# Kernel optimization log

Hardware: AMD Instinct MI355X
Metric: run time of the kernel (lower is better)

## Reference

```python
import jax, jax.numpy as jnp
import numpy as np

H, W = 180, 330
SIZE = 36
K = SIZE + 1  # gaussian patch is 37x37 (arange(-18, 19))
SIGMA = 3.0
XR = (30.0, 31.0)
YR = (120.0, 122.0)
ALPHA = 0.7
EPS = 1e-4


def _conv(x, w, b):
    # 3x3 stride-1 'same' conv, NCHW / OIHW
    y = jax.lax.conv_general_dilated(x, w, (1, 1), 'SAME',
                                     dimension_numbers=('NCHW', 'OIHW', 'NCHW'))
    return y + b[None, :, None, None]


def _bn(x, g, b):
    # eval-mode batchnorm with running_mean=0, running_var=1
    return x * g[None, :, None, None] + b[None, :, None, None]


def _pool(x):
    return jax.lax.reduce_window(x, -jnp.inf, jax.lax.max,
                                 (1, 1, 2, 2), (1, 1, 2, 2), 'VALID')


def _heatmap(x_t):
    # vectorized gaussian splatting (replaces the torch double python loop)
    B, T = x_t.shape[0], x_t.shape[1]
    x_scale = H / (XR[1] - XR[0])
    y_scale = W / (YR[1] - YR[0])
    xp = H - ((x_t[:, :, 0] - XR[0]) * x_scale).astype(jnp.int32)  # [B,T]
    yp = ((x_t[:, :, 1] - YR[0]) * y_scale).astype(jnp.int32)
    valid = ~(jnp.isnan(x_t[:, :, 0]) | jnp.isnan(x_t[:, :, 1]))

    ax = jnp.arange(-(SIZE // 2), SIZE // 2 + 1, dtype=jnp.float32)  # 37
    k1 = jnp.exp(-ax ** 2 / (2.0 * SIGMA ** 2))
    kern = k1[:, None] * k1[None, :]
    kern = kern / kern.sum()  # [K,K]

    xs = jnp.clip(xp - SIZE // 2, 0, H - SIZE)
    xe = jnp.clip(xp + SIZE // 2, 0, H)
    ys = jnp.clip(yp - SIZE // 2, 0, W - SIZE)
    ye = jnp.clip(yp + SIZE // 2, 0, W)

    r = jnp.arange(K)
    # mask = kernel[:ksx, :ksy] selection, matching torch's top-left slicing
    mask = (r[None, None, :, None] < (xe - xs)[:, :, None, None]) \
         & (r[None, None, None, :] < (ye - ys)[:, :, None, None]) \
         & valid[:, :, None, None]
    patch = kern[None, None] * mask  # [B,T,K,K]

    # scatter-add into padded heatmap, then crop
    Hp, Wp = H + K, W + K
    bidx = jnp.arange(B)[:, None, None, None]
    ridx = xs[:, :, None, None] + r[None, None, :, None]
    cidx = ys[:, :, None, None] + r[None, None, None, :]
    idx = (bidx * Hp + ridx) * Wp + cidx  # [B,T,K,K]
    heat = jnp.zeros((B * Hp * Wp,), jnp.float32)
    heat = heat.at[idx.reshape(-1)].add(patch.reshape(-1))
    heat = heat.reshape(B, Hp, Wp)[:, :H, :W]

    m = heat.max(axis=(1, 2), keepdims=True)
    return heat / (m + 1e-10)


def reference(x_t, image_tensor,
              c1_w, c1_b, bn1_g, bn1_b, c2_w, c2_b, bn2_g, bn2_b,
              a1_w, a1_b, abn1_g, abn1_b, a2_w, a2_b, abn2_g, abn2_b,
              p1_w, p1_b, pbn1_g, pbn1_b, p2_w, p2_b, pbn2_g, pbn2_b,
              fc_w, fc_b):
    heat = _heatmap(x_t)
    fused = ALPHA * heat + (1.0 - ALPHA) * image_tensor  # [B,H,W]
    x = fused[:, None]  # [B,1,H,W]

    # features
    x = _pool(jax.nn.relu(_bn(_conv(x, c1_w, c1_b), bn1_g, bn1_b)))   # [B,32,90,165]
    x = _pool(jax.nn.relu(_bn(_conv(x, c2_w, c2_b), bn2_g, bn2_b)))   # [B,64,45,82]

    # add_ons -> f_x
    f = jax.nn.relu(_bn(_conv(x, a1_w, a1_b), abn1_g, abn1_b))
    f_x = jax.nn.sigmoid(_bn(_conv(f, a2_w, a2_b), abn2_g, abn2_b))   # [B,128,45,82]

    # get_p_map: p_map[:-1] (conv,bn,relu,conv,bn) then relu, scale, steep sigmoid
    p = jax.nn.relu(_bn(_conv(x, p1_w, p1_b), pbn1_g, pbn1_b))
    p = jax.nn.relu(_bn(_conv(p, p2_w, p2_b), pbn2_g, pbn2_b))
    p = p - p.min(axis=(1, 2, 3), keepdims=True)
    p = p / jnp.maximum(p.max(axis=(1, 2, 3), keepdims=True), EPS)
    p_map = jax.nn.sigmoid(10.0 * (p - 0.5))                          # [B,128,45,82]

    # attn_map + fc1
    p_size = f_x.shape[2] * f_x.shape[3]
    p_x = jnp.einsum('bphw,bchw->bpc', p_map, f_x) / p_size           # [B,128,128]
    out = p_x.reshape(p_x.shape[0], -1) @ fc_w.T + fc_b               # [B,256]
    return out


def setup_inputs() -> dict:
    key = jax.random.key(0)
    ks = jax.random.split(key, 32)
    B, T = 32, 1024
    u = jax.random.uniform(ks[0], (B, T, 2))
    x_t = jnp.stack([XR[0] + u[..., 0] * (XR[1] - XR[0]),
                     YR[0] + u[..., 1] * (YR[1] - YR[0])], axis=-1)
    image_tensor = jax.random.uniform(ks[1], (B, H, W))

    def w(k, shp):
        return jax.random.normal(k, shp, jnp.float32) * 0.05

    inp = {'x_t': x_t, 'image_tensor': image_tensor,
           'c1_w': w(ks[2], (32, 1, 3, 3)), 'c1_b': w(ks[3], (32,)),
           'bn1_g': jnp.ones((32,)), 'bn1_b': w(ks[4], (32,)),
           'c2_w': w(ks[5], (64, 32, 3, 3)), 'c2_b': w(ks[6], (64,)),
           'bn2_g': jnp.ones((64,)), 'bn2_b': w(ks[7], (64,)),
           'a1_w': w(ks[8], (128, 64, 3, 3)), 'a1_b': w(ks[9], (128,)),
           'abn1_g': jnp.ones((128,)), 'abn1_b': w(ks[10], (128,)),
           'a2_w': w(ks[11], (128, 128, 3, 3)), 'a2_b': w(ks[12], (128,)),
           'abn2_g': jnp.ones((128,)), 'abn2_b': w(ks[13], (128,)),
           'p1_w': w(ks[14], (128, 64, 3, 3)), 'p1_b': w(ks[15], (128,)),
           'pbn1_g': jnp.ones((128,)), 'pbn1_b': w(ks[16], (128,)),
           'p2_w': w(ks[17], (128, 128, 3, 3)), 'p2_b': w(ks[18], (128,)),
           'pbn2_g': jnp.ones((128,)), 'pbn2_b': w(ks[19], (128,)),
           'fc_w': w(ks[20], (256, 16384)), 'fc_b': w(ks[21], (256,))}
    return inp
```

## Files before the change

### kernel.cpp

```cpp
#include <hip/hip_runtime.h>
#include <hip/hip_bf16.h>

#define NB 32
#define NT 1024
#define IH 180
#define IW 330
#define KSZ 37
#define XBINS 181
#define H1 90
#define W1 165
#define H2 45
#define W2 82
#define PIX2 (H2*W2)
#define KTOT PIX2
#define KPAD 3712
#define CH1 32
#define CH2 64
#define CH3 128
#define NSTRIP 6
#define NKC 8

#define NKF 256
#define KCF 64

#define BXR 12
#define YHW 165
#define GROWS_MAX 54

#define EL_HEAT (IH*IW)
#define EL_REGB 237600
#define EL_REGC (CH2*PIX2/2)
#define EL_REGD (CH3*KPAD/2)
#define EL_REGE (CH3*KPAD/2)
#define EL_PX   (CH3*CH3)
#define EL_PER_BATCH (EL_HEAT + EL_REGB + EL_REGC + EL_REGD + EL_REGE + EL_PX)

#define WSH_A1 (9*128*64)
#define WSH_A2 (9*128*128)
#define WSH_C2 (9*64*32)
#define WSH_TOT (2*WSH_A1 + 2*WSH_A2 + WSH_C2)

typedef __attribute__((ext_vector_type(8))) short short8;
typedef __attribute__((ext_vector_type(4))) float floatx4;

__device__ __forceinline__ short f2bf(float v) {
    __hip_bfloat16 h = __float2bfloat16(v);
    return *reinterpret_cast<short*>(&h);
}
__device__ __forceinline__ float b2f(short s) {
    __hip_bfloat16 h = *reinterpret_cast<__hip_bfloat16*>(&s);
    return __bfloat162float(h);
}

__global__ __launch_bounds__(256) void mm_init(unsigned* __restrict__ m_bits,
                                               unsigned* __restrict__ pmm_bits) {
    int i = threadIdx.x;
    if (i < 64) {
        m_bits[i] = 0u;
        pmm_bits[2 * i]     = 0x7F800000u;
        pmm_bits[2 * i + 1] = 0u;
    }
}

__global__ __launch_bounds__(256) void heat_scatter_cols(const float* __restrict__ x_t,
                                                         float* __restrict__ G,
                                                         int b0) {
    const int strip = blockIdx.x;
    const int lb = blockIdx.y;
    const int b = b0 + lb;
    const int c0 = strip * 64;
    const int cw = min(64, IW - c0);
    __shared__ float g[XBINS * 64];
    __shared__ float k1n[64];
    __shared__ float2 pts[NT];
    const int tid = threadIdx.x;

    if (tid < 64) {
        float v = 0.0f;
        if (tid < KSZ) {
            float ax = (float)tid - 18.0f;
            v = expf(-ax * ax / 18.0f);
        }
        k1n[tid] = v;
    }
    for (int i = tid; i < XBINS * 64; i += 256) g[i] = 0.0f;
    {
        const float2* xb = (const float2*)x_t + (size_t)b * NT;
        for (int i = tid; i < NT; i += 256) pts[i] = xb[i];
    }
    __syncthreads();
    if (tid == 0) {
        float s = 0.0f;
        for (int i = 0; i < KSZ; i++) s += k1n[i];
        float inv = 1.0f / s;
        for (int i = 0; i < KSZ; i++) k1n[i] *= inv;
    }
    __syncthreads();

    const int wave = tid >> 6;
    const int lane = tid & 63;
    const float kc = k1n[lane];

    for (int p = wave; p < NT; p += 4) {
        float x = pts[p].x, y = pts[p].y;
        if (isnan(x) || isnan(y)) continue;
        int xp = IH - (int)((x - 30.0f) * 180.0f);
        xp = min(max(xp, 0), 180);
        int yp = (int)((y - 120.0f) * 165.0f);
        int ys = min(max(yp - 18, 0), IW - 36);
        int ye = min(max(yp + 18, 0), IW);
        int nc = ye - ys;
        int col = ys + lane;
        if (lane < nc && col >= c0 && col < c0 + cw)
            atomicAdd(&g[xp * 64 + col - c0], kc);
    }
    __syncthreads();
    for (int i = tid; i < XBINS * cw; i += 256) {
        int row = i / cw, col = i % cw;
        G[((size_t)lb * XBINS + row) * IW + c0 + col] = g[row * 64 + col];
    }
}

__global__ __launch_bounds__(256) void heat_rowcombine(const float* __restrict__ G,
                                                       float* __restrict__ heat,
                                                       unsigned* __restrict__ m_bits) {
    const int band = blockIdx.x;
    const int lb = blockIdx.y;
    const int half = blockIdx.z;
    const int X0 = band * BXR;
    const int c0 = half * YHW;
    const int tid = threadIdx.x;

    __shared__ float k1n[64];
    __shared__ float gs[GROWS_MAX * YHW];
    __shared__ float red[256];

    if (tid < 64) {
        float v = 0.0f;
        if (tid < KSZ) {
            float ax = (float)tid - 18.0f;
            v = expf(-ax * ax / 18.0f);
        }
        k1n[tid] = v;
    }

    const int rlo = max(0, X0 - 17);
    const int rhi = (X0 + BXR - 1 >= IH - 36) ? 180 : (X0 + BXR - 1 + 18);
    const int nrows = rhi - rlo + 1;
    const float* Gb = G + (size_t)lb * XBINS * IW;
    for (int i = tid; i < nrows * YHW; i += 256) {
        int r = i / YHW, y = i % YHW;
        gs[i] = Gb[(size_t)(rlo + r) * IW + c0 + y];
    }
    __syncthreads();
    if (tid == 0) {
        float s = 0.0f;
        for (int i = 0; i < KSZ; i++) s += k1n[i];
        float inv = 1.0f / s;
        for (int i = 0; i < KSZ; i++) k1n[i] *= inv;
    }
    __syncthreads();

    float lmax = 0.0f;
    for (int p = tid; p < BXR * YHW; p += 256) {
        const int xr = p / YHW;
        const int yy = p % YHW;
        const int X = X0 + xr;
        const int Y = c0 + yy;
        const int lo = max(0, X - 17);
        const int hi = (X >= IH - 36) ? 180 : X + 18;
        float s = 0.0f;
        for (int xp = lo; xp <= hi; ++xp) {
            int xs = min(max(xp - 18, 0), IH - 36);
            s += k1n[X - xs] * gs[(xp - rlo) * YHW + yy];
        }
        heat[(size_t)lb * EL_HEAT + (size_t)X * IW + Y] = s;
        lmax = fmaxf(lmax, s);
    }
    red[tid] = lmax;
    __syncthreads();
    for (int st = 128; st > 0; st >>= 1) {
        if (tid < st) red[tid] = fmaxf(red[tid], red[tid + st]);
        __syncthreads();
    }
    if (tid == 0) atomicMax(&m_bits[lb], __float_as_uint(red[0]));
}

__global__ __launch_bounds__(256) void conv1_pool(const float* __restrict__ heat,
                                                  const float* __restrict__ image,
                                                  const float* __restrict__ m,
                                                  const float* __restrict__ w,
                                                  const float* __restrict__ cb,
                                                  const float* __restrict__ g,
                                                  const float* __restrict__ bb,
                                                  short* __restrict__ out1,
                                                  int b0, int gb) {
    __shared__ float ws_[CH1 * 9];
    __shared__ float bs_[CH1];
    const int tid = threadIdx.x;
    for (int i = tid; i < CH1 * 9; i += 256) {
        int oc = i / 9;
        ws_[i] = w[i] * g[oc];
    }
    if (tid < CH1) bs_[tid] = cb[tid] * g[tid] + bb[tid];
    __syncthreads();

    int t = blockIdx.x * 256 + tid;
    if (t >= gb * H1 * W1) return;
    int lb = t / (H1 * W1);
    int r = t % (H1 * W1);
    int py = r / W1, px = r % W1;
    const float s = 0.7f / (m[lb] + 1e-10f);
    const float* hb = heat + (size_t)lb * EL_HEAT;
    const float* ib = image + (size_t)(b0 + lb) * EL_HEAT;

    float v[4][4];
    int y0 = 2 * py - 1, x0 = 2 * px - 1;
#pragma unroll
    for (int i = 0; i < 4; i++) {
#pragma unroll
        for (int j = 0; j < 4; j++) {
            int y = y0 + i, x = x0 + j;
            float val = 0.0f;
            if (y >= 0 && y < IH && x >= 0 && x < IW) {
                size_t idx = (size_t)y * IW + x;
                val = s * hb[idx] + 0.3f * ib[idx];
            }
            v[i][j] = val;
        }
    }
    short8 pk[4];
#pragma unroll
    for (int oc = 0; oc < CH1; oc++) {
        float a00 = 0, a01 = 0, a10 = 0, a11 = 0;
        const float* wp = &ws_[oc * 9];
#pragma unroll
        for (int ky = 0; ky < 3; ky++) {
#pragma unroll
            for (int kx = 0; kx < 3; kx++) {
                float wv = wp[ky * 3 + kx];
                a00 += wv * v[ky][kx];
                a01 += wv * v[ky][kx + 1];
                a10 += wv * v[ky + 1][kx];
                a11 += wv * v[ky + 1][kx + 1];
            }
        }
        float bias = bs_[oc];
        a00 = fmaxf(a00 + bias, 0.0f);
        a01 = fmaxf(a01 + bias, 0.0f);
        a10 = fmaxf(a10 + bias, 0.0f);
        a11 = fmaxf(a11 + bias, 0.0f);
        pk[oc >> 3][oc & 7] = f2bf(fmaxf(fmaxf(a00, a01), fmaxf(a10, a11)));
    }
    short8* op = reinterpret_cast<short8*>(&out1[((size_t)lb * H1 * W1 + r) * CH1]);
#pragma unroll
    for (int vv = 0; vv < 4; vv++) op[vv] = pk[vv];
}

__global__ __launch_bounds__(256) void wfold_k(const float* __restrict__ w,
                                               const float* __restrict__ g,
                                               const float* __restrict__ cb,
                                               const float* __restrict__ bb,
                                               short* __restrict__ wT,
                                               float* __restrict__ bfold,
                                               int OC, int IC) {
    int i = blockIdx.x * 256 + threadIdx.x;
    int n = 9 * OC * IC;
    if (i >= n) return;
    int tap = i / (OC * IC);
    int r = i % (OC * IC);
    int oc = r / IC;
    int ic = r % IC;
    wT[i] = f2bf(w[((size_t)oc * IC + ic) * 9 + tap] * g[oc]);
    if (tap == 0 && ic == 0) bfold[oc] = cb[oc] * g[oc] + bb[oc];
}

__global__ __launch_bounds__(256) void conv2_mfma(const short* __restrict__ in,
                                                  const short* __restrict__ wT,
                                                  const float* __restrict__ bfold,
                                                  short* __restrict__ out) {
    const int xt = blockIdx.x;
    const int yt = blockIdx.y;
    const int lb = blockIdx.z;
    const int x0 = xt * 32, y0 = yt * 8;
    const int tid = threadIdx.x;
    const int wave = tid >> 6, lane = tid & 63;
    const int mm = lane & 15, q = lane >> 4;
    constexpr int AP = 40;
    constexpr int CP = 72;
    __shared__ __align__(16) short smem[10 * 34 * AP];

    floatx4 acc[2][2][4];
#pragma unroll
    for (int a = 0; a < 2; ++a)
#pragma unroll
        for (int bq = 0; bq < 2; ++bq)
#pragma unroll
            for (int j = 0; j < 4; ++j) acc[a][bq][j] = (floatx4){0.f, 0.f, 0.f, 0.f};

    const short* inb = in + (size_t)lb * (H1 * W1) * CH1;
    for (int e = tid; e < 10 * 34 * 4; e += 256) {
        int dy = e / (34 * 4);
        int r = e % (34 * 4);
        int tx = r / 4;
        int i8 = r % 4;
        int yin = y0 + dy - 1, xin = x0 + tx - 1;
        short8 hv = {0, 0, 0, 0, 0, 0, 0, 0};
        if (yin >= 0 && yin < H1 && xin >= 0 && xin < W1)
            hv = *reinterpret_cast<const short8*>(&inb[((size_t)(yin * W1 + xin)) * CH1 + i8 * 8]);
        *reinterpret_cast<short8*>(&smem[(dy * 34 + tx) * AP + i8 * 8]) = hv;
    }
    __syncthreads();

#pragma unroll
    for (int tap = 0; tap < 9; ++tap) {
        const int dy = tap / 3, dx = tap % 3;
        short8 bf[4];
#pragma unroll
        for (int j = 0; j < 4; ++j)
            bf[j] = *reinterpret_cast<const short8*>(&wT[((size_t)tap * 64 + j * 16 + mm) * 32 + q * 8]);
#pragma unroll
        for (int row = 0; row < 2; ++row) {
#pragma unroll
            for (int xh = 0; xh < 2; ++xh) {
                short8 af = *reinterpret_cast<const short8*>(
                    &smem[((2 * wave + row + dy) * 34 + xh * 16 + dx + mm) * AP + q * 8]);
#pragma unroll
                for (int j = 0; j < 4; ++j)
                    acc[row][xh][j] = __builtin_amdgcn_mfma_f32_16x16x32_bf16(af, bf[j], acc[row][xh][j], 0, 0, 0);
            }
        }
    }
    __syncthreads();

    short* cst = smem;
#pragma unroll
    for (int xh = 0; xh < 2; ++xh) {
#pragma unroll
        for (int j = 0; j < 4; ++j) {
            const float bias = bfold[j * 16 + mm];
#pragma unroll
            for (int rp = 0; rp < 2; ++rp) {
                int pxl = xh * 8 + q * 2 + rp;
                float v = fmaxf(fmaxf(acc[0][xh][j][2 * rp], acc[0][xh][j][2 * rp + 1]),
                                fmaxf(acc[1][xh][j][2 * rp], acc[1][xh][j][2 * rp + 1]));
                v = fmaxf(v + bias, 0.0f);
                cst[(wave * 16 + pxl) * CP + j * 16 + mm] = f2bf(v);
            }
        }
    }
    __syncthreads();

    short* ob = out + (size_t)lb * PIX2 * CH2;
    for (int e = tid; e < 512; e += 256) {
        int pl = e >> 3, c8 = e & 7;
        int py = yt * 4 + (pl >> 4);
        int pxg = xt * 16 + (pl & 15);
        if (py < H2 && pxg < W2)
            *reinterpret_cast<short8*>(&ob[((size_t)py * W2 + pxg) * CH2 + c8 * 8]) =
                *reinterpret_cast<const short8*>(&cst[pl * CP + c8 * 8]);
    }
}

template <int IC, bool SIG, int OM>
__global__ __launch_bounds__(256) void conv3x3_mfma(const short* __restrict__ in,
                                                    const short* __restrict__ wT,
                                                    const float* __restrict__ bfold,
                                                    short* __restrict__ outp) {
    const int xt = blockIdx.x;
    const int yt = blockIdx.y;
    const int lb = blockIdx.z;
    const int x0 = xt * 32, y0 = yt * 4;
    const int tid = threadIdx.x;
    const int wave = tid >> 6, lane = tid & 63;
    const int mm = lane & 15, q = lane >> 4;

    constexpr int KC = 32;
    constexpr int NCH = IC / KC;
    constexpr int AP = 40;
    constexpr int CP0 = 136;
    constexpr int CP2 = 132;
    __shared__ __align__(16) short smem[17408];

    floatx4 acc[16];
#pragma unroll
    for (int i = 0; i < 16; ++i) acc[i] = (floatx4){0.f, 0.f, 0.f, 0.f};

    const short* inb = in + (size_t)lb * PIX2 * IC;

    for (int c = 0; c < NCH; ++c) {
        const int ic0 = c * KC;
        for (int e = tid; e < 6 * 34 * (KC / 8); e += 256) {
            int dy = e / (34 * (KC / 8));
            int r  = e % (34 * (KC / 8));
            int tx = r / (KC / 8);
            int i8 = r % (KC / 8);
            int yin = y0 + dy - 1, xin = x0 + tx - 1;
            short8 hv = {0, 0, 0, 0, 0, 0, 0, 0};
            if (yin >= 0 && yin < H2 && xin >= 0 && xin < W2)
                hv = *reinterpret_cast<const short8*>(
                    &inb[((size_t)(yin * W2 + xin)) * IC + ic0 + i8 * 8]);
            *reinterpret_cast<short8*>(&smem[(dy * 34 + tx) * AP + i8 * 8]) = hv;
        }
        __syncthreads();

        const int oc0 = wave * 32 + mm;
#pragma unroll
        for (int tap = 0; tap < 9; ++tap) {
            const int dy = tap / 3, dx = tap % 3;
            short8 b0 = *reinterpret_cast<const short8*>(
                &wT[((size_t)tap * 128 + oc0) * IC + ic0 + q * 8]);
            short8 b1 = *reinterpret_cast<const short8*>(
                &wT[((size_t)tap * 128 + oc0 + 16) * IC + ic0 + q * 8]);
#pragma unroll
            for (int t = 0; t < 8; ++t) {
                const int tr = t >> 1, tc = t & 1;
                short8 af = *reinterpret_cast<const short8*>(
                    &smem[((tr + dy) * 34 + tc * 16 + dx + mm) * AP + q * 8]);
                acc[t * 2]     = __builtin_amdgcn_mfma_f32_16x16x32_bf16(af, b0, acc[t * 2], 0, 0, 0);
                acc[t * 2 + 1] = __builtin_amdgcn_mfma_f32_16x16x32_bf16(af, b1, acc[t * 2 + 1], 0, 0, 0);
            }
        }
        __syncthreads();
    }

    const int oc0 = wave * 32 + mm;
    const float bias0 = bfold[oc0];
    const float bias1 = bfold[oc0 + 16];
    short* cst = smem;
#pragma unroll
    for (int t = 0; t < 8; ++t) {
        const int tr = t >> 1, tc = t & 1;
#pragma unroll
        for (int r = 0; r < 4; ++r) {
            int pl = tr * 32 + tc * 16 + q * 4 + r;
            float z0 = acc[t * 2][r] + bias0;
            float z1 = acc[t * 2 + 1][r] + bias1;
            if (SIG) {
                z0 = 1.0f / (1.0f + expf(-z0));
                z1 = 1.0f / (1.0f + expf(-z1));
            } else {
                z0 = fmaxf(z0, 0.0f);
                z1 = fmaxf(z1, 0.0f);
            }
            if (OM == 0) {
                cst[pl * CP0 + oc0] = f2bf(z0);
                cst[pl * CP0 + oc0 + 16] = f2bf(z1);
            } else {
                cst[oc0 * CP2 + pl] = f2bf(z0);
                cst[(oc0 + 16) * CP2 + pl] = f2bf(z1);
            }
        }
    }
    __syncthreads();

    if (OM == 0) {
        short* ob = outp + (size_t)lb * PIX2 * 128;
        for (int e = tid; e < 2048; e += 256) {
            int pl = e >> 4, c8 = e & 15;
            int yy = y0 + (pl >> 5), xx = x0 + (pl & 31);
            if (yy < H2 && xx < W2)
                *reinterpret_cast<short8*>(&ob[((size_t)yy * W2 + xx) * 128 + c8 * 8]) =
                    *reinterpret_cast<const short8*>(&cst[pl * CP0 + c8 * 8]);
        }
    } else {
        short* ob = outp + (size_t)lb * 128 * KPAD;
        for (int e = tid; e < 8192; e += 256) {
            int oc = e >> 6;
            int r2 = e & 63;
            int yy4 = r2 >> 4;
            int x2 = (r2 & 15) * 2;
            int yy = y0 + yy4, xx = x0 + x2;
            if (yy < H2 && xx < W2) {
                int pl = yy4 * 32 + x2;
                if (xx + 1 < W2) {
                    *reinterpret_cast<int*>(&ob[(size_t)oc * KPAD + yy * W2 + xx]) =
                        *reinterpret_cast<const int*>(&cst[oc * CP2 + pl]);
                } else {
                    ob[(size_t)oc * KPAD + yy * W2 + xx] = cst[oc * CP2 + pl];
                }
            }
        }
    }
}

__global__ __launch_bounds__(256) void pminmax(const short* __restrict__ p,
                                               unsigned* __restrict__ pmm_bits) {
    const int c = blockIdx.x;
    const int lb = blockIdx.y;
    const short* pb = p + (size_t)lb * 128 * KPAD + (size_t)c * KPAD;
    float mn = INFINITY, mx = 0.0f;
    for (int i = threadIdx.x; i < PIX2; i += 256) {
        float v = b2f(pb[i]);
        mn = fminf(mn, v);
        mx = fmaxf(mx, v);
    }
    __shared__ float rmn[256], rmx[256];
    rmn[threadIdx.x] = mn; rmx[threadIdx.x] = mx;
    __syncthreads();
    for (int s = 128; s > 0; s >>= 1) {
        if (threadIdx.x < s) {
            rmn[threadIdx.x] = fminf(rmn[threadIdx.x], rmn[threadIdx.x + s]);
            rmx[threadIdx.x] = fmaxf(rmx[threadIdx.x], rmx[threadIdx.x + s]);
        }
        __syncthreads();
    }
    if (threadIdx.x == 0) {
        atomicMin(&pmm_bits[lb * 2],     __float_as_uint(rmn[0]));
        atomicMax(&pmm_bits[lb * 2 + 1], __float_as_uint(rmx[0]));
    }
}

__global__ __launch_bounds__(256) void einsum_part(const short* __restrict__ pp2,
                                                   const short* __restrict__ fxb,
                                                   const float* __restrict__ mm_,
                                                   float* __restrict__ px_part) {
    const int kc = blockIdx.x;
    const int lb = blockIdx.y;
    const int gb = gridDim.y;
    const int tid = threadIdx.x;
    const int wave = tid >> 6, lane = tid & 63;
    const int mm = lane & 15, q = lane >> 4;
    constexpr int AP = 72;
    __shared__ __align__(16) short As[128 * AP];
    __shared__ __align__(16) short Bs[128 * AP];

    const float mn = mm_[lb * 2];
    const float denom = fmaxf(mm_[lb * 2 + 1] - mn, 1e-4f);
    const float rden = 1.0f / denom;

    floatx4 acc[2][8];
#pragma unroll
    for (int a = 0; a < 2; ++a)
#pragma unroll
        for (int n = 0; n < 8; ++n) acc[a][n] = (floatx4){0.f, 0.f, 0.f, 0.f};

    const short* Ab = pp2 + (size_t)lb * 128 * KPAD;
    const short* Bb = fxb + (size_t)lb * 128 * KPAD;

    for (int it = 0; it < 8; ++it) {
        const int kk = kc * 512 + it * 64;
        if (kk >= KTOT) break;
        for (int e = tid; e < 2048; e += 256) {
            const bool isA = (e < 1024);
            const int e2 = isA ? e : e - 1024;
            const int row = e2 >> 3, i8 = e2 & 7;
            const int k = kk + i8 * 8;
            const short* src = (isA ? Ab : Bb) + (size_t)row * KPAD + k;
            short8 v = {0, 0, 0, 0, 0, 0, 0, 0};
            if (k + 8 <= KTOT) {
                v = *reinterpret_cast<const short8*>(src);
            } else {
#pragma unroll
                for (int j = 0; j < 8; ++j) v[j] = (k + j < KTOT) ? src[j] : (short)0;
            }
            if (isA) {
#pragma unroll
                for (int j = 0; j < 8; ++j) {
                    if (k + j < KTOT) {
                        float f = (b2f(v[j]) - mn) * rden;
                        v[j] = f2bf(1.0f / (1.0f + expf(-10.0f * (f - 0.5f))));
                    } else v[j] = 0;
                }
                *reinterpret_cast<short8*>(&As[row * AP + i8 * 8]) = v;
            } else {
                *reinterpret_cast<short8*>(&Bs[row * AP + i8 * 8]) = v;
            }
        }
        __syncthreads();
#pragma unroll
        for (int ks = 0; ks < 2; ++ks) {
            short8 af0 = *reinterpret_cast<const short8*>(&As[((2 * wave) * 16 + mm) * AP + ks * 32 + q * 8]);
            short8 af1 = *reinterpret_cast<const short8*>(&As[((2 * wave + 1) * 16 + mm) * AP + ks * 32 + q * 8]);
#pragma unroll
            for (int n = 0; n < 8; ++n) {
                short8 bf = *reinterpret_cast<const short8*>(&Bs[(n * 16 + mm) * AP + ks * 32 + q * 8]);
                acc[0][n] = __builtin_amdgcn_mfma_f32_16x16x32_bf16(af0, bf, acc[0][n], 0, 0, 0);
                acc[1][n] = __builtin_amdgcn_mfma_f32_16x16x32_bf16(af1, bf, acc[1][n], 0, 0, 0);
            }
        }
        __syncthreads();
    }

    float* base = px_part + ((size_t)kc * gb + lb) * EL_PX;
#pragma unroll
    for (int a = 0; a < 2; ++a) {
        const int gm0 = (2 * wave + a) * 16 + q * 4;
#pragma unroll
        for (int n = 0; n < 8; ++n) {
            const int gn = n * 16 + mm;
#pragma unroll
            for (int r = 0; r < 4; ++r)
                base[(size_t)(gm0 + r) * 128 + gn] = acc[a][n][r];
        }
    }
}

__global__ __launch_bounds__(256) void px_reduce(const float* __restrict__ part,
                                                 float* __restrict__ px,
                                                 int gb) {
    int i = blockIdx.x * 256 + threadIdx.x;
    if (i >= gb * EL_PX) return;
    int lb = i / EL_PX;
    int r = i % EL_PX;
    float s = 0.0f;
#pragma unroll
    for (int kc = 0; kc < NKC; ++kc)
        s += part[((size_t)kc * gb + lb) * EL_PX + r];
    px[i] = s * (1.0f / (float)KTOT);
}

__global__ __launch_bounds__(256) void fc_wt(const float* __restrict__ w,
                                             float* __restrict__ wT) {
    __shared__ float t[32][33];
    const int bk = blockIdx.x * 32;
    const int bo = blockIdx.y * 32;
    const int tx = threadIdx.x & 31;
    const int ty = threadIdx.x >> 5;
#pragma unroll
    for (int r = 0; r < 4; ++r) {
        int o = bo + ty + r * 8;
        t[ty + r * 8][tx] = w[(size_t)o * EL_PX + bk + tx];
    }
    __syncthreads();
#pragma unroll
    for (int r = 0; r < 4; ++r) {
        int k = bk + ty + r * 8;
        wT[(size_t)k * 256 + bo + tx] = t[tx][ty + r * 8];
    }
}

__global__ __launch_bounds__(256) void fc_part(const float* __restrict__ px,
                                               const float* __restrict__ wT,
                                               float* __restrict__ part) {
    const int kc = blockIdx.x;
    const int o = threadIdx.x;
    const int k0 = kc * KCF;
    float acc[32];
#pragma unroll
    for (int lb = 0; lb < 32; ++lb) acc[lb] = 0.0f;

    for (int k8 = 0; k8 < KCF; k8 += 8) {
        float wv[8];
#pragma unroll
        for (int j = 0; j < 8; ++j)
            wv[j] = wT[(size_t)(k0 + k8 + j) * 256 + o];
#pragma unroll
        for (int lb = 0; lb < 32; ++lb) {
            const float* pc = px + (size_t)lb * EL_PX + k0 + k8;
            float4 p0 = *reinterpret_cast<const float4*>(pc);
            float4 p1 = *reinterpret_cast<const float4*>(pc + 4);
            acc[lb] += wv[0] * p0.x + wv[1] * p0.y + wv[2] * p0.z + wv[3] * p0.w
                     + wv[4] * p1.x + wv[5] * p1.y + wv[6] * p1.z + wv[7] * p1.w;
        }
    }
    float* pb = part + (size_t)kc * (32 * 256);
#pragma unroll
    for (int lb = 0; lb < 32; ++lb)
        pb[lb * 256 + o] = acc[lb];
}

__global__ __launch_bounds__(256) void fc_out(const float* __restrict__ part,
                                              const float* __restrict__ fcb,
                                              float* __restrict__ out) {
    const int i = blockIdx.x * 256 + threadIdx.x;
    float s = 0.0f;
    for (int c = 0; c < NKF; ++c)
        s += part[(size_t)c * 8192 + i];
    out[i] = s + fcb[i & 255];
}

__global__ __launch_bounds__(256) void fc_k(const float* __restrict__ px,
                                            const float* __restrict__ w,
                                            const float* __restrict__ bias,
                                            float* __restrict__ out,
                                            int b0) {
    const int gw = blockIdx.x * 4 + (threadIdx.x >> 6);
    const int lane = threadIdx.x & 63;
    const int lb = gw >> 8;
    const int o = gw & 255;
    const float* xb = px + (size_t)lb * EL_PX;
    const float* wr = w + (size_t)o * EL_PX;
    float s = 0.0f;
    for (int k = lane; k < EL_PX; k += 64) s += xb[k] * wr[k];
#pragma unroll
    for (int off = 32; off > 0; off >>= 1) s += __shfl_down(s, off);
    if (lane == 0) out[(size_t)(b0 + lb) * 256 + o] = s + bias[o];
}

extern "C" void kernel_launch(void* const* d_in, const int* in_sizes, int n_in,
                              void* d_out, int out_size, void* d_ws, size_t ws_size,
                              hipStream_t stream) {
    const float* x_t   = (const float*)d_in[0];
    const float* image = (const float*)d_in[1];
    const float* c1_w  = (const float*)d_in[2];
    const float* c1_b  = (const float*)d_in[3];
    const float* bn1_g = (const float*)d_in[4];
    const float* bn1_b = (const float*)d_in[5];
    const float* c2_w  = (const float*)d_in[6];
    const float* c2_b  = (const float*)d_in[7];
    const float* bn2_g = (const float*)d_in[8];
    const float* bn2_b = (const float*)d_in[9];
    const float* a1_w  = (const float*)d_in[10];
    const float* a1_b  = (const float*)d_in[11];
    const float* abn1_g= (const float*)d_in[12];
    const float* abn1_b= (const float*)d_in[13];
    const float* a2_w  = (const float*)d_in[14];
    const float* a2_b  = (const float*)d_in[15];
    const float* abn2_g= (const float*)d_in[16];
    const float* abn2_b= (const float*)d_in[17];
    const float* p1_w  = (const float*)d_in[18];
    const float* p1_b  = (const float*)d_in[19];
    const float* pbn1_g= (const float*)d_in[20];
    const float* pbn1_b= (const float*)d_in[21];
    const float* p2_w  = (const float*)d_in[22];
    const float* p2_b  = (const float*)d_in[23];
    const float* pbn2_g= (const float*)d_in[24];
    const float* pbn2_b= (const float*)d_in[25];
    const float* fc_w  = (const float*)d_in[26];
    const float* fc_b  = (const float*)d_in[27];
    float* outp = (float*)d_out;

    float* ws = (float*)d_ws;
    short* wTa1 = (short*)ws;
    short* wTa2 = wTa1 + WSH_A1;
    short* wTp1 = wTa2 + WSH_A2;
    short* wTp2 = wTp1 + WSH_A1;
    short* wTc2 = wTp2 + WSH_A2;
    float* bfa1 = ws + WSH_TOT / 2;
    float* bfa2 = bfa1 + 128;
    float* bfp1 = bfa2 + 128;
    float* bfp2 = bfp1 + 128;
    float* bfc2 = bfp2 + 128;
    float* dyn  = bfc2 + 128;
    const size_t fixed_floats = WSH_TOT / 2 + 1024;

    int GB = 32;
    while (GB > 1) {
        size_t need = ((size_t)GB * EL_PER_BATCH + fixed_floats + 256) * sizeof(float);
        if (need <= ws_size) break;
        GB >>= 1;
    }
    const int ngroups = NB / GB;

    float* heat = dyn;
    float* m    = heat + (size_t)GB * EL_HEAT;
    float* regB = m + 64;
    float* regC = regB + (size_t)GB * EL_REGB;
    float* regD = regC + (size_t)GB * EL_REGC;
    float* regE = regD + (size_t)GB * EL_REGD;
    float* pmm  = regE + (size_t)GB * EL_REGE;
    float* px   = pmm + 128;

    float* G      = regD;
    short* out1b  = (short*)regB;
    short* out2b  = (short*)regC;
    short* fbuf   = (short*)regD;
    short* fxbf   = (short*)regE;
    short* pp1    = (short*)regB;
    short* pp2    = (short*)regD;
    float* pxpart = regB;
    float* fcwT   = regD;
    float* fcpart = regB;

    wfold_k<<<(9 * 128 * CH2 + 255) / 256, 256, 0, stream>>>(a1_w, abn1_g, a1_b, abn1_b, wTa1, bfa1, 128, CH2);
    wfold_k<<<(9 * 128 * CH3 + 255) / 256, 256, 0, stream>>>(a2_w, abn2_g, a2_b, abn2_b, wTa2, bfa2, 128, CH3);
    wfold_k<<<(9 * 128 * CH2 + 255) / 256, 256, 0, stream>>>(p1_w, pbn1_g, p1_b, pbn1_b, wTp1, bfp1, 128, CH2);
    wfold_k<<<(9 * 128 * CH3 + 255) / 256, 256, 0, stream>>>(p2_w, pbn2_g, p2_b, pbn2_b, wTp2, bfp2, 128, CH3);
    wfold_k<<<(9 * 64 * 32 + 255) / 256, 256, 0, stream>>>(c2_w, bn2_g, c2_b, bn2_b, wTc2, bfc2, 64, 32);

    for (int gidx = 0; gidx < ngroups; ++gidx) {
        const int b0 = gidx * GB;
        mm_init<<<1, 256, 0, stream>>>((unsigned*)m, (unsigned*)pmm);
        heat_scatter_cols<<<dim3(NSTRIP, GB), 256, 0, stream>>>(x_t, G, b0);
        heat_rowcombine<<<dim3(IH / BXR, GB, 2), 256, 0, stream>>>(G, heat, (unsigned*)m);
        conv1_pool<<<(GB * H1 * W1 + 255) / 256, 256, 0, stream>>>(
            heat, image, m, c1_w, c1_b, bn1_g, bn1_b, out1b, b0, GB);
        conv2_mfma<<<dim3(6, 12, GB), 256, 0, stream>>>(out1b, wTc2, bfc2, out2b);
        conv3x3_mfma<CH2, false, 0><<<dim3(3, 12, GB), 256, 0, stream>>>(out2b, wTa1, bfa1, fbuf);
        conv3x3_mfma<CH3, true,  2><<<dim3(3, 12, GB), 256, 0, stream>>>(fbuf, wTa2, bfa2, fxbf);
        conv3x3_mfma<CH2, false, 0><<<dim3(3, 12, GB), 256, 0, stream>>>(out2b, wTp1, bfp1, pp1);
        conv3x3_mfma<CH3, false, 2><<<dim3(3, 12, GB), 256, 0, stream>>>(pp1, wTp2, bfp2, pp2);
        pminmax<<<dim3(128, GB), 256, 0, stream>>>(pp2, (unsigned*)pmm);
        einsum_part<<<dim3(NKC, GB), 256, 0, stream>>>(pp2, fxbf, pmm, pxpart);
        px_reduce<<<(GB * EL_PX + 255) / 256, 256, 0, stream>>>(pxpart, px, GB);
        if (GB == 32) {
            fc_wt<<<dim3(EL_PX / 32, 256 / 32), 256, 0, stream>>>(fc_w, fcwT);
            fc_part<<<NKF, 256, 0, stream>>>(px, fcwT, fcpart);
            fc_out<<<8192 / 256, 256, 0, stream>>>(fcpart, fc_b, outp);
        } else {
            fc_k<<<GB * 64, 256, 0, stream>>>(px, fc_w, fc_b, outp, b0);
        }
    }
}
```

Before: 673.3 us.

## Split conv3x3 output channels across blocks and merge twin first-stage convs

Rewrites the 3x3 MFMA conv so each block computes 64 of the 128 output channels, and each wave computes one output row against four weight fragments instead of all rows against two. This doubles the grid (and quadruples it for the merged launch), cuts accumulator registers from 16 to 8 floatx4 and halves shared memory, which should raise occupancy. The two convolutions that read the same input (a1 and p1) are fused into one dual-weight launch, saving a kernel launch. The cost is that the input tile is now loaded into shared memory once per channel half, roughly doubling input halo traffic.

```diff
diff --git a/kernel.cpp b/kernel.cpp
--- a/kernel.cpp
+++ b/kernel.cpp
@@ -362,29 +362,41 @@
     }
 }
 
-template <int IC, bool SIG, int OM>
-__global__ __launch_bounds__(256) void conv3x3_mfma(const short* __restrict__ in,
-                                                    const short* __restrict__ wT,
-                                                    const float* __restrict__ bfold,
-                                                    short* __restrict__ outp) {
+template <int IC, bool SIG, int OM, bool DUAL>
+__global__ __launch_bounds__(256) void conv3x3_v2(const short* __restrict__ in,
+                                                  const short* __restrict__ wA,
+                                                  const short* __restrict__ wB,
+                                                  const float* __restrict__ bA,
+                                                  const float* __restrict__ bB,
+                                                  short* __restrict__ oA,
+                                                  short* __restrict__ oB) {
     const int xt = blockIdx.x;
-    const int yt = blockIdx.y;
+    const int yt = blockIdx.y % 12;
+    const int och = blockIdx.y / 12;
     const int lb = blockIdx.z;
     const int x0 = xt * 32, y0 = yt * 4;
     const int tid = threadIdx.x;
     const int wave = tid >> 6, lane = tid & 63;
     const int mm = lane & 15, q = lane >> 4;
 
+    const short* wT = wA;
+    const float* bfold = bA;
+    short* outp = oA;
+    if (DUAL && och >= 2) { wT = wB; bfold = bB; outp = oB; }
+    const int ocbase = (DUAL ? (och & 1) : och) * 64;
+
     constexpr int KC = 32;
     constexpr int NCH = IC / KC;
     constexpr int AP = 40;
-    constexpr int CP0 = 136;
+    constexpr int CP0 = 72;
     constexpr int CP2 = 132;
-    __shared__ __align__(16) short smem[17408];
-
-    floatx4 acc[16];
-#pragma unroll
-    for (int i = 0; i < 16; ++i) acc[i] = (floatx4){0.f, 0.f, 0.f, 0.f};
+    __shared__ __align__(16) short smem[9216];
+
+    floatx4 acc[2][4];
+#pragma unroll
+    for (int tc = 0; tc < 2; ++tc)
+#pragma unroll
+        for (int j = 0; j < 4; ++j) acc[tc][j] = (floatx4){0.f, 0.f, 0.f, 0.f};
 
     const short* inb = in + (size_t)lb * PIX2 * IC;
 
@@ -404,51 +416,42 @@
         }
         __syncthreads();
 
-        const int oc0 = wave * 32 + mm;
 #pragma unroll
         for (int tap = 0; tap < 9; ++tap) {
             const int dy = tap / 3, dx = tap % 3;
-            short8 b0 = *reinterpret_cast<const short8*>(
-                &wT[((size_t)tap * 128 + oc0) * IC + ic0 + q * 8]);
-            short8 b1 = *reinterpret_cast<const short8*>(
-                &wT[((size_t)tap * 128 + oc0 + 16) * IC + ic0 + q * 8]);
-#pragma unroll
-            for (int t = 0; t < 8; ++t) {
-                const int tr = t >> 1, tc = t & 1;
+            short8 bf[4];
+#pragma unroll
+            for (int j = 0; j < 4; ++j)
+                bf[j] = *reinterpret_cast<const short8*>(
+                    &wT[((size_t)tap * 128 + ocbase + j * 16 + mm) * IC + ic0 + q * 8]);
+#pragma unroll
+            for (int tc = 0; tc < 2; ++tc) {
                 short8 af = *reinterpret_cast<const short8*>(
-                    &smem[((tr + dy) * 34 + tc * 16 + dx + mm) * AP + q * 8]);
-                acc[t * 2]     = __builtin_amdgcn_mfma_f32_16x16x32_bf16(af, b0, acc[t * 2], 0, 0, 0);
-                acc[t * 2 + 1] = __builtin_amdgcn_mfma_f32_16x16x32_bf16(af, b1, acc[t * 2 + 1], 0, 0, 0);
+                    &smem[((wave + dy) * 34 + tc * 16 + dx + mm) * AP + q * 8]);
+#pragma unroll
+                for (int j = 0; j < 4; ++j)
+                    acc[tc][j] = __builtin_amdgcn_mfma_f32_16x16x32_bf16(af, bf[j], acc[tc][j], 0, 0, 0);
             }
         }
         __syncthreads();
     }
 
-    const int oc0 = wave * 32 + mm;
-    const float bias0 = bfold[oc0];
-    const float bias1 = bfold[oc0 + 16];
+    float biasv[4];
+#pragma unroll
+    for (int j = 0; j < 4; ++j) biasv[j] = bfold[ocbase + j * 16 + mm];
     short* cst = smem;
 #pragma unroll
-    for (int t = 0; t < 8; ++t) {
-        const int tr = t >> 1, tc = t & 1;
-#pragma unroll
-        for (int r = 0; r < 4; ++r) {
-            int pl = tr * 32 + tc * 16 + q * 4 + r;
-            float z0 = acc[t * 2][r] + bias0;
-            float z1 = acc[t * 2 + 1][r] + bias1;
-            if (SIG) {
-                z0 = 1.0f / (1.0f + expf(-z0));
-                z1 = 1.0f / (1.0f + expf(-z1));
-            } else {
-                z0 = fmaxf(z0, 0.0f);
-                z1 = fmaxf(z1, 0.0f);
-            }
-            if (OM == 0) {
-                cst[pl * CP0 + oc0] = f2bf(z0);
-                cst[pl * CP0 + oc0 + 16] = f2bf(z1);
-            } else {
-                cst[oc0 * CP2 + pl] = f2bf(z0);
-                cst[(oc0 + 16) * CP2 + pl] = f2bf(z1);
+    for (int tc = 0; tc < 2; ++tc) {
+#pragma unroll
+        for (int j = 0; j < 4; ++j) {
+#pragma unroll
+            for (int r = 0; r < 4; ++r) {
+                int pl = wave * 32 + tc * 16 + q * 4 + r;
+                float z = acc[tc][j][r] + biasv[j];
+                if (SIG) z = 1.0f / (1.0f + expf(-z));
+                else z = fmaxf(z, 0.0f);
+                if (OM == 0) cst[pl * CP0 + j * 16 + mm] = f2bf(z);
+                else cst[(j * 16 + mm) * CP2 + pl] = f2bf(z);
             }
         }
     }
@@ -456,28 +459,29 @@
 
     if (OM == 0) {
         short* ob = outp + (size_t)lb * PIX2 * 128;
-        for (int e = tid; e < 2048; e += 256) {
-            int pl = e >> 4, c8 = e & 15;
+        for (int e = tid; e < 1024; e += 256) {
+            int pl = e >> 3, c8 = e & 7;
             int yy = y0 + (pl >> 5), xx = x0 + (pl & 31);
             if (yy < H2 && xx < W2)
-                *reinterpret_cast<short8*>(&ob[((size_t)yy * W2 + xx) * 128 + c8 * 8]) =
+                *reinterpret_cast<short8*>(&ob[((size_t)yy * W2 + xx) * 128 + ocbase + c8 * 8]) =
                     *reinterpret_cast<const short8*>(&cst[pl * CP0 + c8 * 8]);
         }
     } else {
         short* ob = outp + (size_t)lb * 128 * KPAD;
-        for (int e = tid; e < 8192; e += 256) {
-            int oc = e >> 6;
+        for (int e = tid; e < 4096; e += 256) {
+            int ocl = e >> 6;
             int r2 = e & 63;
             int yy4 = r2 >> 4;
             int x2 = (r2 & 15) * 2;
             int yy = y0 + yy4, xx = x0 + x2;
             if (yy < H2 && xx < W2) {
                 int pl = yy4 * 32 + x2;
+                int oc = ocbase + ocl;
                 if (xx + 1 < W2) {
                     *reinterpret_cast<int*>(&ob[(size_t)oc * KPAD + yy * W2 + xx]) =
-                        *reinterpret_cast<const int*>(&cst[oc * CP2 + pl]);
+                        *reinterpret_cast<const int*>(&cst[ocl * CP2 + pl]);
                 } else {
-                    ob[(size_t)oc * KPAD + yy * W2 + xx] = cst[oc * CP2 + pl];
+                    ob[(size_t)oc * KPAD + yy * W2 + xx] = cst[ocl * CP2 + pl];
                 }
             }
         }
@@ -777,10 +781,12 @@
         conv1_pool<<<(GB * H1 * W1 + 255) / 256, 256, 0, stream>>>(
             heat, image, m, c1_w, c1_b, bn1_g, bn1_b, out1b, b0, GB);
         conv2_mfma<<<dim3(6, 12, GB), 256, 0, stream>>>(out1b, wTc2, bfc2, out2b);
-        conv3x3_mfma<CH2, false, 0><<<dim3(3, 12, GB), 256, 0, stream>>>(out2b, wTa1, bfa1, fbuf);
-        conv3x3_mfma<CH3, true,  2><<<dim3(3, 12, GB), 256, 0, stream>>>(fbuf, wTa2, bfa2, fxbf);
-        conv3x3_mfma<CH2, false, 0><<<dim3(3, 12, GB), 256, 0, stream>>>(out2b, wTp1, bfp1, pp1);
-        conv3x3_mfma<CH3, false, 2><<<dim3(3, 12, GB), 256, 0, stream>>>(pp1, wTp2, bfp2, pp2);
+        conv3x3_v2<CH2, false, 0, true><<<dim3(3, 48, GB), 256, 0, stream>>>(
+            out2b, wTa1, wTp1, bfa1, bfp1, fbuf, pp1);
+        conv3x3_v2<CH3, true,  2, false><<<dim3(3, 24, GB), 256, 0, stream>>>(
+            fbuf, wTa2, wTa2, bfa2, bfa2, fxbf, fxbf);
+        conv3x3_v2<CH3, false, 2, false><<<dim3(3, 24, GB), 256, 0, stream>>>(
+            pp1, wTp2, wTp2, bfp2, bfp2, pp2, pp2);
         pminmax<<<dim3(128, GB), 256, 0, stream>>>(pp2, (unsigned*)pmm);
         einsum_part<<<dim3(NKC, GB), 256, 0, stream>>>(pp2, fxbf, pmm, pxpart);
         px_reduce<<<(GB * EL_PX + 255) / 256, 256, 0, stream>>>(pxpart, px, GB);
```

New measurement: 980.5 us. 1.46x slower.

## Halve conv LDS footprint with two-pass epilogue and prefetch tap weights

Applied to the files above, without the earlier changes.

Shrinks the conv3x3 MFMA kernel's shared memory from 17408 to 8704 shorts. The output staging epilogue is split into two halves (pixel halves for NHWC output, channel halves for the planar output), each separated by barriers. It also software-pipelines the per-tap weight loads from global memory one tap ahead of the MFMA loop. The aim is more resident blocks per CU and less latency exposure on weight fetches, at the cost of extra barriers and higher register pressure in the epilogue.

```diff
diff --git a/kernel.cpp b/kernel.cpp
--- a/kernel.cpp
+++ b/kernel.cpp
@@ -380,13 +380,14 @@
     constexpr int AP = 40;
     constexpr int CP0 = 136;
     constexpr int CP2 = 132;
-    __shared__ __align__(16) short smem[17408];
+    __shared__ __align__(16) short smem[8704];
 
     floatx4 acc[16];
 #pragma unroll
     for (int i = 0; i < 16; ++i) acc[i] = (floatx4){0.f, 0.f, 0.f, 0.f};
 
     const short* inb = in + (size_t)lb * PIX2 * IC;
+    const int oc0 = wave * 32 + mm;
 
     for (int c = 0; c < NCH; ++c) {
         const int ic0 = c * KC;
@@ -404,82 +405,116 @@
         }
         __syncthreads();
 
-        const int oc0 = wave * 32 + mm;
+        const short* wpb = &wT[((size_t)oc0) * IC + ic0 + q * 8];
+        const size_t tstr = (size_t)128 * IC;
+        short8 b0c = *reinterpret_cast<const short8*>(wpb);
+        short8 b1c = *reinterpret_cast<const short8*>(wpb + (size_t)16 * IC);
 #pragma unroll
         for (int tap = 0; tap < 9; ++tap) {
+            short8 b0n = b0c, b1n = b1c;
+            if (tap < 8) {
+                const short* wn = wpb + (size_t)(tap + 1) * tstr;
+                b0n = *reinterpret_cast<const short8*>(wn);
+                b1n = *reinterpret_cast<const short8*>(wn + (size_t)16 * IC);
+            }
             const int dy = tap / 3, dx = tap % 3;
-            short8 b0 = *reinterpret_cast<const short8*>(
-                &wT[((size_t)tap * 128 + oc0) * IC + ic0 + q * 8]);
-            short8 b1 = *reinterpret_cast<const short8*>(
-                &wT[((size_t)tap * 128 + oc0 + 16) * IC + ic0 + q * 8]);
 #pragma unroll
             for (int t = 0; t < 8; ++t) {
                 const int tr = t >> 1, tc = t & 1;
                 short8 af = *reinterpret_cast<const short8*>(
                     &smem[((tr + dy) * 34 + tc * 16 + dx + mm) * AP + q * 8]);
-                acc[t * 2]     = __builtin_amdgcn_mfma_f32_16x16x32_bf16(af, b0, acc[t * 2], 0, 0, 0);
-                acc[t * 2 + 1] = __builtin_amdgcn_mfma_f32_16x16x32_bf16(af, b1, acc[t * 2 + 1], 0, 0, 0);
-            }
+                acc[t * 2]     = __builtin_amdgcn_mfma_f32_16x16x32_bf16(af, b0c, acc[t * 2], 0, 0, 0);
+                acc[t * 2 + 1] = __builtin_amdgcn_mfma_f32_16x16x32_bf16(af, b1c, acc[t * 2 + 1], 0, 0, 0);
+            }
+            b0c = b0n; b1c = b1n;
         }
         __syncthreads();
     }
 
-    const int oc0 = wave * 32 + mm;
     const float bias0 = bfold[oc0];
     const float bias1 = bfold[oc0 + 16];
     short* cst = smem;
-#pragma unroll
-    for (int t = 0; t < 8; ++t) {
-        const int tr = t >> 1, tc = t & 1;
-#pragma unroll
-        for (int r = 0; r < 4; ++r) {
-            int pl = tr * 32 + tc * 16 + q * 4 + r;
-            float z0 = acc[t * 2][r] + bias0;
-            float z1 = acc[t * 2 + 1][r] + bias1;
-            if (SIG) {
-                z0 = 1.0f / (1.0f + expf(-z0));
-                z1 = 1.0f / (1.0f + expf(-z1));
-            } else {
-                z0 = fmaxf(z0, 0.0f);
-                z1 = fmaxf(z1, 0.0f);
-            }
-            if (OM == 0) {
-                cst[pl * CP0 + oc0] = f2bf(z0);
-                cst[pl * CP0 + oc0 + 16] = f2bf(z1);
-            } else {
-                cst[oc0 * CP2 + pl] = f2bf(z0);
-                cst[(oc0 + 16) * CP2 + pl] = f2bf(z1);
-            }
-        }
-    }
-    __syncthreads();
 
     if (OM == 0) {
         short* ob = outp + (size_t)lb * PIX2 * 128;
-        for (int e = tid; e < 2048; e += 256) {
-            int pl = e >> 4, c8 = e & 15;
-            int yy = y0 + (pl >> 5), xx = x0 + (pl & 31);
-            if (yy < H2 && xx < W2)
-                *reinterpret_cast<short8*>(&ob[((size_t)yy * W2 + xx) * 128 + c8 * 8]) =
-                    *reinterpret_cast<const short8*>(&cst[pl * CP0 + c8 * 8]);
+#pragma unroll
+        for (int h = 0; h < 2; ++h) {
+#pragma unroll
+            for (int t2 = 0; t2 < 4; ++t2) {
+                const int t = 4 * h + t2;
+                const int tr = t >> 1, tc = t & 1;
+#pragma unroll
+                for (int r = 0; r < 4; ++r) {
+                    int pll = (tr & 1) * 32 + tc * 16 + q * 4 + r;
+                    float z0 = acc[t * 2][r] + bias0;
+                    float z1 = acc[t * 2 + 1][r] + bias1;
+                    if (SIG) {
+                        z0 = 1.0f / (1.0f + expf(-z0));
+                        z1 = 1.0f / (1.0f + expf(-z1));
+                    } else {
+                        z0 = fmaxf(z0, 0.0f);
+                        z1 = fmaxf(z1, 0.0f);
+                    }
+                    cst[pll * CP0 + oc0] = f2bf(z0);
+                    cst[pll * CP0 + oc0 + 16] = f2bf(z1);
+                }
+            }
+            __syncthreads();
+            for (int e = tid; e < 1024; e += 256) {
+                int pll = e >> 4, c8 = e & 15;
+                int plg = h * 64 + pll;
+                int yy = y0 + (plg >> 5), xx = x0 + (plg & 31);
+                if (yy < H2 && xx < W2)
+                    *reinterpret_cast<short8*>(&ob[((size_t)yy * W2 + xx) * 128 + c8 * 8]) =
+                        *reinterpret_cast<const short8*>(&cst[pll * CP0 + c8 * 8]);
+            }
+            __syncthreads();
         }
     } else {
         short* ob = outp + (size_t)lb * 128 * KPAD;
-        for (int e = tid; e < 8192; e += 256) {
-            int oc = e >> 6;
-            int r2 = e & 63;
-            int yy4 = r2 >> 4;
-            int x2 = (r2 & 15) * 2;
-            int yy = y0 + yy4, xx = x0 + x2;
-            if (yy < H2 && xx < W2) {
-                int pl = yy4 * 32 + x2;
-                if (xx + 1 < W2) {
-                    *reinterpret_cast<int*>(&ob[(size_t)oc * KPAD + yy * W2 + xx]) =
-                        *reinterpret_cast<const int*>(&cst[oc * CP2 + pl]);
-                } else {
-                    ob[(size_t)oc * KPAD + yy * W2 + xx] = cst[oc * CP2 + pl];
+#pragma unroll
+        for (int h = 0; h < 2; ++h) {
+            if ((wave >> 1) == h) {
+                const int ocl = (wave & 1) * 32 + mm;
+#pragma unroll
+                for (int t = 0; t < 8; ++t) {
+                    const int tr = t >> 1, tc = t & 1;
+#pragma unroll
+                    for (int r = 0; r < 4; ++r) {
+                        int pl = tr * 32 + tc * 16 + q * 4 + r;
+                        float z0 = acc[t * 2][r] + bias0;
+                        float z1 = acc[t * 2 + 1][r] + bias1;
+                        if (SIG) {
+                            z0 = 1.0f / (1.0f + expf(-z0));
+                            z1 = 1.0f / (1.0f + expf(-z1));
+                        } else {
+                            z0 = fmaxf(z0, 0.0f);
+                            z1 = fmaxf(z1, 0.0f);
+                        }
+                        cst[ocl * CP2 + pl] = f2bf(z0);
+                        cst[(ocl + 16) * CP2 + pl] = f2bf(z1);
+                    }
                 }
             }
+            __syncthreads();
+            for (int e = tid; e < 4096; e += 256) {
+                int ocl = e >> 6;
+                int oc = 64 * h + ocl;
+                int r2 = e & 63;
+                int yy4 = r2 >> 4;
+                int x2 = (r2 & 15) * 2;
+                int yy = y0 + yy4, xx = x0 + x2;
+                if (yy < H2 && xx < W2) {
+                    int pl = yy4 * 32 + x2;
+                    if (xx + 1 < W2) {
+                        *reinterpret_cast<int*>(&ob[(size_t)oc * KPAD + yy * W2 + xx]) =
+                            *reinterpret_cast<const int*>(&cst[ocl * CP2 + pl]);
+                    } else {
+                        ob[(size_t)oc * KPAD + yy * W2 + xx] = cst[ocl * CP2 + pl];
+                    }
+                }
+            }
+            __syncthreads();
         }
     }
 }
```

Result: slower. 697.9 us (+3.7%).
